# Performance work log

Hardware: AMD Instinct MI355X
Metric: run time of the kernel (lower is better)

Reference implementation:

```python
import jax, jax.numpy as jnp
import numpy as np

D_HIDDEN = 1024
N_HEADS = 16
D_HEAD = 64
B, N = 4, 1024
EPS = 1e-5


def _lin(x, w, b):
    # torch Linear: y = x @ W^T + b, w: [out, in]
    return jnp.einsum('...i,oi->...o', x, w) + b


def _ln(x, g, b):
    m = jnp.mean(x, axis=-1, keepdims=True)
    v = jnp.mean(jnp.square(x - m), axis=-1, keepdims=True)
    return (x - m) * jax.lax.rsqrt(v + EPS) * g + b


def setup_inputs() -> dict:
    key = jax.random.key(0)
    ks = jax.random.split(key, 20)
    d = D_HIDDEN
    s = 0.02
    inp = {
        'x': jax.random.normal(ks[0], (B, N, d), jnp.float32),
        'time_emb': jax.random.normal(ks[1], (B, d), jnp.float32),
        'ln1_g': jnp.ones((d,), jnp.float32),
        'ln1_b': jnp.zeros((d,), jnp.float32),
        's1_w': jax.random.normal(ks[2], (d, d), jnp.float32) * s,
        's1_b': jnp.zeros((d,), jnp.float32),
        'o1_w': jax.random.normal(ks[3], (d, d), jnp.float32) * s,
        'o1_b': jnp.zeros((d,), jnp.float32),
        'qkv_w': jax.random.normal(ks[4], (3 * d, d), jnp.float32) * s,
        'qkv_b': jnp.zeros((3 * d,), jnp.float32),
        'proj_w': jax.random.normal(ks[5], (d, d), jnp.float32) * s,
        'proj_b': jnp.zeros((d,), jnp.float32),
        'ln2_g': jnp.ones((d,), jnp.float32),
        'ln2_b': jnp.zeros((d,), jnp.float32),
        's2_w': jax.random.normal(ks[6], (d, d), jnp.float32) * s,
        's2_b': jnp.zeros((d,), jnp.float32),
        'o2_w': jax.random.normal(ks[7], (d, d), jnp.float32) * s,
        'o2_b': jnp.zeros((d,), jnp.float32),
        'up_w': jax.random.normal(ks[8], (4 * d, d), jnp.float32) * s,
        'up_b': jnp.zeros((4 * d,), jnp.float32),
        'down_w': jax.random.normal(ks[9], (d, 4 * d), jnp.float32) * s,
        'down_b': jnp.zeros((d,), jnp.float32),
    }
    return inp


def reference(x, time_emb, ln1_g, ln1_b, s1_w, s1_b, o1_w, o1_b,
              qkv_w, qkv_b, proj_w, proj_b, ln2_g, ln2_b,
              s2_w, s2_b, o2_w, o2_b, up_w, up_b, down_w, down_b):
    d = D_HIDDEN

    def ada(h, sw, sb, ow, ob):
        scale = _lin(time_emb, sw, sb)[:, None, :]   # [B,1,d]
        offset = _lin(time_emb, ow, ob)[:, None, :]
        return (1.0 + scale) * h + offset

    # attention branch
    h = ada(_ln(x, ln1_g, ln1_b), s1_w, s1_b, o1_w, o1_b)
    qkv = _lin(h, qkv_w, qkv_b)                       # [B,N,3d]
    q, k, v = jnp.split(qkv, 3, axis=-1)
    q = q.reshape(B, N, N_HEADS, D_HEAD)
    k = k.reshape(B, N, N_HEADS, D_HEAD)
    v = v.reshape(B, N, N_HEADS, D_HEAD)
    wei = jnp.einsum('bnhd,bmhd->bhnm', q, k) * (D_HEAD ** -0.5)
    wei = jax.nn.softmax(wei, axis=-1)
    attn = jnp.einsum('bhnm,bmhd->bnhd', wei, v).reshape(B, N, d)
    x = x + _lin(attn, proj_w, proj_b)

    # mlp branch (torch nn.GELU default = exact erf gelu)
    h = ada(_ln(x, ln2_g, ln2_b), s2_w, s2_b, o2_w, o2_b)
    h = jax.nn.gelu(_lin(h, up_w, up_b), approximate=False)
    x = x + _lin(h, down_w, down_b)
    return x, time_emb
```

## Files before the change

kernel.cpp:

```cpp
#include <hip/hip_runtime.h>
#include <hip/hip_bf16.h>
#include <math.h>

#define DH 1024
#define BB 4
#define NN 1024
#define NH 16
#define HD 64

typedef __attribute__((ext_vector_type(8))) short bf16x8;
typedef __attribute__((ext_vector_type(4))) float f32x4;
typedef unsigned short u16;

static __device__ __forceinline__ u16 f2bf(float f) {
  __hip_bfloat16 h = __float2bfloat16(f);
  return *reinterpret_cast<u16*>(&h);
}

#define MFMA16(a, b, c) __builtin_amdgcn_mfma_f32_16x16x32_bf16(a, b, c, 0, 0, 0)
#define VMCNT(n) asm volatile("s_waitcnt vmcnt(" #n ")" ::: "memory")
#define MEMFENCE asm volatile("" ::: "memory")

static __device__ __forceinline__ void async16(const void* g, void* l) {
  __builtin_amdgcn_global_load_lds(
      (const __attribute__((address_space(1))) void*)g,
      (__attribute__((address_space(3))) void*)l, 16, 0, 0);
}

__global__ void cvt_all_kernel(const float* __restrict__ wq, const float* __restrict__ wp,
                               const float* __restrict__ wu, const float* __restrict__ wd,
                               u16* __restrict__ oq, u16* __restrict__ op,
                               u16* __restrict__ ou, u16* __restrict__ od) {
  int i = blockIdx.x * 256 + threadIdx.x;
  const float* src; u16* dst; int off;
  if (i < 786432)            { src = wq; dst = oq; off = i; }
  else if (i < 1048576)      { src = wp; dst = op; off = i - 786432; }
  else if (i < 2097152)      { src = wu; dst = ou; off = i - 1048576; }
  else                       { src = wd; dst = od; off = i - 2097152; }
  float4 v = reinterpret_cast<const float4*>(src)[off];
  ushort4 o;
  o.x = f2bf(v.x); o.y = f2bf(v.y); o.z = f2bf(v.z); o.w = f2bf(v.w);
  reinterpret_cast<ushort4*>(dst)[off] = o;
}

__global__ __launch_bounds__(256) void adaln_kernel(
    const float* __restrict__ e,
    const float* __restrict__ w_s1, const float* __restrict__ b_s1,
    const float* __restrict__ w_o1, const float* __restrict__ b_o1,
    const float* __restrict__ w_s2, const float* __restrict__ b_s2,
    const float* __restrict__ w_o2, const float* __restrict__ b_o2,
    float* __restrict__ out) {
  int tid = threadIdx.x, wid = tid >> 6, lane = tid & 63;
  int mat = blockIdx.y;
  const float* w; const float* bs; float addc;
  if (mat == 0)      { w = w_s1; bs = b_s1; addc = 1.f; }
  else if (mat == 1) { w = w_o1; bs = b_o1; addc = 0.f; }
  else if (mat == 2) { w = w_s2; bs = b_s2; addc = 1.f; }
  else               { w = w_o2; bs = b_o2; addc = 0.f; }
  int col = blockIdx.x * 4 + wid;
  float a0 = 0.f, a1 = 0.f, a2 = 0.f, a3 = 0.f;
  const float* wc_ = w + (size_t)col * DH;
  for (int i = 0; i < 16; ++i) {
    int k = i * 64 + lane;
    float wv = wc_[k];
    a0 += wv * e[k];
    a1 += wv * e[DH + k];
    a2 += wv * e[2 * DH + k];
    a3 += wv * e[3 * DH + k];
  }
  #pragma unroll
  for (int msk = 32; msk; msk >>= 1) {
    a0 += __shfl_xor(a0, msk); a1 += __shfl_xor(a1, msk);
    a2 += __shfl_xor(a2, msk); a3 += __shfl_xor(a3, msk);
  }
  if (lane == 0) {
    float bb = bs[col] + addc;
    out[mat * (4 * DH) + 0 * DH + col] = a0 + bb;
    out[mat * (4 * DH) + 1 * DH + col] = a1 + bb;
    out[mat * (4 * DH) + 2 * DH + col] = a2 + bb;
    out[mat * (4 * DH) + 3 * DH + col] = a3 + bb;
  }
}

__global__ __launch_bounds__(256) void ln_mod_kernel(
    const float* __restrict__ x, const float* __restrict__ g, const float* __restrict__ bta,
    const float* __restrict__ sp, const float* __restrict__ off, u16* __restrict__ out) {
  int row = blockIdx.x;
  int b = row >> 10;
  int tid = threadIdx.x;
  int wid = tid >> 6, lane = tid & 63;
  const float4 xv = reinterpret_cast<const float4*>(x + (size_t)row * DH)[tid];
  float s = xv.x + xv.y + xv.z + xv.w;
  float ss = xv.x * xv.x + xv.y * xv.y + xv.z * xv.z + xv.w * xv.w;
  #pragma unroll
  for (int m = 32; m; m >>= 1) { s += __shfl_xor(s, m); ss += __shfl_xor(ss, m); }
  __shared__ float red[8];
  if (lane == 0) { red[wid] = s; red[4 + wid] = ss; }
  __syncthreads();
  s = red[0] + red[1] + red[2] + red[3];
  ss = red[4] + red[5] + red[6] + red[7];
  float mean = s * (1.f / DH);
  float var = ss * (1.f / DH) - mean * mean;
  float rstd = rsqrtf(var + 1e-5f);
  int c = tid * 4;
  const float* spb = sp + b * DH + c;
  const float* offb = off + b * DH + c;
  float y0 = (xv.x - mean) * rstd * g[c + 0] + bta[c + 0];
  float y1 = (xv.y - mean) * rstd * g[c + 1] + bta[c + 1];
  float y2 = (xv.z - mean) * rstd * g[c + 2] + bta[c + 2];
  float y3 = (xv.w - mean) * rstd * g[c + 3] + bta[c + 3];
  ushort4 o;
  o.x = f2bf(spb[0] * y0 + offb[0]);
  o.y = f2bf(spb[1] * y1 + offb[1]);
  o.z = f2bf(spb[2] * y2 + offb[2]);
  o.w = f2bf(spb[3] * y3 + offb[3]);
  reinterpret_cast<ushort4*>(out + (size_t)row * DH)[tid] = o;
}

enum { EPI_BF16 = 0, EPI_GELU = 1, EPI_F32PART = 2 };

template <int EPI>
__global__ __launch_bounds__(512, 2) void gemm256_kernel(
    const u16* __restrict__ A, const u16* __restrict__ W,
    const float* __restrict__ bias, void* __restrict__ outp,
    int N, int K, int KT) {
  extern __shared__ u16 lds[];
  u16* Ab = lds;
  u16* Bb = lds + 32768;
  int tid = threadIdx.x;
  int wid = tid >> 6, lane = tid & 63;
  int l15 = lane & 15, l4 = lane >> 4;
  int wr = wid >> 2, wc = wid & 3;

  int nwg = gridDim.x * gridDim.y;
  int lin = blockIdx.y * gridDim.x + blockIdx.x;
  int q8 = nwg >> 3;
  int lin2 = (lin & 7) * q8 + (lin >> 3);
  int bx = lin2 % gridDim.x, by = lin2 / gridDim.x;
  int m0 = by * 256, n0 = bx * 256;
  int k0 = blockIdx.z * (KT << 5);

  f32x4 acc[8][4] = {};

  const u16* Abase = A + (size_t)m0 * K + k0;
  const u16* Wbase = W + (size_t)n0 * K + k0;
  int i0 = tid, i1 = 512 + tid;
  int r0 = i0 >> 2, c0 = (i0 & 3) ^ ((r0 >> 1) & 3);
  int r1 = i1 >> 2, c1 = (i1 & 3) ^ ((r1 >> 1) & 3);
  size_t gO0 = (size_t)r0 * K + c0 * 8;
  size_t gO1 = (size_t)r1 * K + c1 * 8;
  int lb0 = (wid * 64) * 8;
  int lb1 = (512 + wid * 64) * 8;

  auto stage = [&](int tt) {
    int q = (tt & 3) * 8192;
    const u16* Ak = Abase + tt * 32;
    const u16* Wk = Wbase + tt * 32;
    async16(Ak + gO0, &Ab[q + lb0]);
    async16(Ak + gO1, &Ab[q + lb1]);
    async16(Wk + gO0, &Bb[q + lb0]);
    async16(Wk + gO1, &Bb[q + lb1]);
  };

  auto compute = [&](int tt) {
    int q = (tt & 3) * 8192;
    bf16x8 af[8], bfr[4];
    #pragma unroll
    for (int m = 0; m < 8; ++m) {
      int row = wr * 128 + m * 16 + l15;
      int ps = l4 ^ ((row >> 1) & 3);
      af[m] = *reinterpret_cast<const bf16x8*>(&Ab[q + row * 32 + ps * 8]);
    }
    #pragma unroll
    for (int n = 0; n < 4; ++n) {
      int row = wc * 64 + n * 16 + l15;
      int ps = l4 ^ ((row >> 1) & 3);
      bfr[n] = *reinterpret_cast<const bf16x8*>(&Bb[q + row * 32 + ps * 8]);
    }
    #pragma unroll
    for (int m = 0; m < 8; ++m)
      #pragma unroll
      for (int n = 0; n < 4; ++n)
        acc[m][n] = MFMA16(af[m], bfr[n], acc[m][n]);
  };

  stage(0);
  if (KT > 1) stage(1);
  if (KT > 2) stage(2);
  for (int t = 0; t < KT; ++t) {
    if (t < KT - 3) { stage(t + 3); VMCNT(12); }
    else if (t == KT - 3) { VMCNT(8); }
    else if (t == KT - 2) { VMCNT(4); }
    else { VMCNT(0); }
    __builtin_amdgcn_s_barrier();
    MEMFENCE;
    compute(t);
    MEMFENCE;
    __builtin_amdgcn_s_barrier();
  }

  int M = gridDim.y * 256;
  float* fout = (float*)outp + (size_t)blockIdx.z * M * N;
  #pragma unroll
  for (int n = 0; n < 4; ++n) {
    int col = n0 + wc * 64 + n * 16 + l15;
    float bv = (EPI == EPI_F32PART) ? 0.f : bias[col];
    #pragma unroll
    for (int m = 0; m < 8; ++m) {
      #pragma unroll
      for (int r = 0; r < 4; ++r) {
        int rowg = m0 + wr * 128 + m * 16 + l4 * 4 + r;
        float v = acc[m][n][r] + bv;
        if (EPI == EPI_GELU) {
          v = 0.5f * v * (1.f + erff(v * 0.70710678118f));
          ((u16*)outp)[(size_t)rowg * N + col] = f2bf(v);
        } else if (EPI == EPI_BF16) {
          ((u16*)outp)[(size_t)rowg * N + col] = f2bf(v);
        } else {
          fout[(size_t)rowg * N + col] = v;
        }
      }
    }
  }
}

enum { OEPI_BF16 = 0, OEPI_GELU = 1, OEPI_RES = 2 };

template <int EPI>
__global__ __launch_bounds__(256, 3) void gemm_bt_kernel(
    const u16* __restrict__ A, const u16* __restrict__ W,
    const float* __restrict__ bias, const float* __restrict__ resid,
    void* __restrict__ outp, int N, int K) {
  __shared__ __align__(16) u16 As[2][128 * 32];
  __shared__ __align__(16) u16 Ws[2][128 * 32];
  int tid = threadIdx.x;
  int wid = tid >> 6, lane = tid & 63;
  int l15 = lane & 15, l4 = lane >> 4;
  int m0 = blockIdx.y * 128, n0 = blockIdx.x * 128;
  int wr = wid >> 1, wc = wid & 1;
  f32x4 acc[4][4] = {};

  const int KT = K >> 5;
  int idx0 = tid, idx1 = 256 + tid;
  int rowA0 = idx0 >> 2, gs0 = (idx0 & 3) ^ ((rowA0 >> 1) & 3);
  int rowA1 = idx1 >> 2, gs1 = (idx1 & 3) ^ ((rowA1 >> 1) & 3);
  const u16* Abase = A + (size_t)m0 * K;
  const u16* Wbase = W + (size_t)n0 * K;
  int lb0 = (wid * 64) * 8;
  int lb1 = (256 + wid * 64) * 8;

  auto stage = [&](int buf, int kt) {
    const u16* Ak = Abase + kt * 32;
    const u16* Wk = Wbase + kt * 32;
    async16(Ak + (size_t)rowA0 * K + gs0 * 8, &As[buf][lb0]);
    async16(Wk + (size_t)rowA0 * K + gs0 * 8, &Ws[buf][lb0]);
    async16(Ak + (size_t)rowA1 * K + gs1 * 8, &As[buf][lb1]);
    async16(Wk + (size_t)rowA1 * K + gs1 * 8, &Ws[buf][lb1]);
  };

  auto compute = [&](int buf) {
    bf16x8 af[4], wf[4];
    #pragma unroll
    for (int m = 0; m < 4; ++m) {
      int row = wr * 64 + m * 16 + l15;
      int ps = l4 ^ ((row >> 1) & 3);
      af[m] = *reinterpret_cast<const bf16x8*>(&As[buf][row * 32 + ps * 8]);
    }
    #pragma unroll
    for (int n = 0; n < 4; ++n) {
      int row = wc * 64 + n * 16 + l15;
      int ps = l4 ^ ((row >> 1) & 3);
      wf[n] = *reinterpret_cast<const bf16x8*>(&Ws[buf][row * 32 + ps * 8]);
    }
    #pragma unroll
    for (int m = 0; m < 4; ++m)
      #pragma unroll
      for (int n = 0; n < 4; ++n)
        acc[m][n] = MFMA16(af[m], wf[n], acc[m][n]);
  };

  stage(0, 0);
  __syncthreads();
  int buf = 0;
  for (int kt = 0; kt < KT - 1; ++kt) {
    stage(buf ^ 1, kt + 1);
    compute(buf);
    __syncthreads();
    buf ^= 1;
  }
  compute(buf);

  #pragma unroll
  for (int n = 0; n < 4; ++n) {
    int col = n0 + wc * 64 + n * 16 + l15;
    float bv = bias[col];
    #pragma unroll
    for (int m = 0; m < 4; ++m) {
      #pragma unroll
      for (int r = 0; r < 4; ++r) {
        int rowg = m0 + wr * 64 + m * 16 + l4 * 4 + r;
        float v = acc[m][n][r] + bv;
        if (EPI == OEPI_GELU) {
          v = 0.5f * v * (1.f + erff(v * 0.70710678118f));
          ((u16*)outp)[(size_t)rowg * N + col] = f2bf(v);
        } else if (EPI == OEPI_BF16) {
          ((u16*)outp)[(size_t)rowg * N + col] = f2bf(v);
        } else {
          ((float*)outp)[(size_t)rowg * N + col] = v + resid[(size_t)rowg * N + col];
        }
      }
    }
  }
}

__global__ __launch_bounds__(256) void reduce4_kernel(
    const float* __restrict__ part, const float* __restrict__ x2,
    const float* __restrict__ bias, float* __restrict__ out) {
  size_t i = (size_t)blockIdx.x * 256 + threadIdx.x;
  const size_t MN4 = (size_t)4096 * 1024 / 4;
  float4 a0 = reinterpret_cast<const float4*>(part)[i];
  float4 a1 = reinterpret_cast<const float4*>(part)[i + MN4];
  float4 a2 = reinterpret_cast<const float4*>(part)[i + 2 * MN4];
  float4 a3 = reinterpret_cast<const float4*>(part)[i + 3 * MN4];
  float4 xr = reinterpret_cast<const float4*>(x2)[i];
  int col = (int)((i * 4) & 1023);
  float4 bv = *reinterpret_cast<const float4*>(&bias[col]);
  float4 o;
  o.x = xr.x + bv.x + a0.x + a1.x + a2.x + a3.x;
  o.y = xr.y + bv.y + a0.y + a1.y + a2.y + a3.y;
  o.z = xr.z + bv.z + a0.z + a1.z + a2.z + a3.z;
  o.w = xr.w + bv.w + a0.w + a1.w + a2.w + a3.w;
  reinterpret_cast<float4*>(out)[i] = o;
}

__global__ __launch_bounds__(256, 4) void attn_kernel(
    const u16* __restrict__ qkv, u16* __restrict__ out) {
  __shared__ __align__(16) u16 Ks[2][4096];
  __shared__ __align__(16) u16 Vt[2][4096];
  __shared__ __align__(16) u16 Ps[4][1024];
  int tid = threadIdx.x, wid = tid >> 6, lane = tid & 63;
  int l15 = lane & 15, l4 = lane >> 4;
  int L = blockIdx.y * gridDim.x + blockIdx.x;
  int qt = (L >> 3) & 15;
  int bh = (L & 7) | ((L >> 7) << 3);
  int b = bh >> 4, h = bh & 15;
  const size_t SN = 3 * DH;
  const u16* qb = qkv + (size_t)b * NN * SN + h * HD;
  const u16* kb = qb + DH;
  const u16* vb = qb + 2 * DH;

  int qrow = qt * 64 + wid * 16 + l15;
  bf16x8 qf[2];
  #pragma unroll
  for (int ks = 0; ks < 2; ++ks)
    qf[ks] = *reinterpret_cast<const bf16x8*>(qb + (size_t)qrow * SN + ks * 32 + l4 * 8);

  float m_[4], l_[4];
  f32x4 o_[4] = {};
  #pragma unroll
  for (int r = 0; r < 4; ++r) { m_[r] = -1e30f; l_[r] = 0.f; }

  int iA = tid, iB = 256 + tid;
  int jA = iA >> 3, sA = iA & 7, gsA = sA ^ (jA & 7);
  int jB = iB >> 3, sB = iB & 7, gsB = sB ^ (jB & 7);

  auto vwrite = [&](int bufn, bf16x8 v0, bf16x8 v1) {
    #pragma unroll
    for (int e = 0; e < 8; ++e) {
      int d = sA * 8 + e;
      int ps = (jA >> 3) ^ (d & 7) ^ ((d >> 3) & 7);
      Vt[bufn][d * 64 + ps * 8 + (jA & 7)] = v0[e];
      int d2 = sB * 8 + e;
      int ps2 = (jB >> 3) ^ (d2 & 7) ^ ((d2 >> 3) & 7);
      Vt[bufn][d2 * 64 + ps2 * 8 + (jB & 7)] = v1[e];
    }
  };

  {
    async16(kb + (size_t)jA * SN + gsA * 8, &Ks[0][iA * 8]);
    async16(kb + (size_t)jB * SN + gsB * 8, &Ks[0][iB * 8]);
    bf16x8 v0 = *reinterpret_cast<const bf16x8*>(vb + (size_t)jA * SN + sA * 8);
    bf16x8 v1 = *reinterpret_cast<const bf16x8*>(vb + (size_t)jB * SN + sB * 8);
    vwrite(0, v0, v1);
    __syncthreads();
  }

  int buf = 0;
  for (int t = 0; t < 16; ++t) {
    bf16x8 vna, vnb;
    if (t < 15) {
      const u16* kt = kb + (size_t)(t + 1) * 64 * SN;
      const u16* vt = vb + (size_t)(t + 1) * 64 * SN;
      async16(kt + (size_t)jA * SN + gsA * 8, &Ks[buf ^ 1][iA * 8]);
      async16(kt + (size_t)jB * SN + gsB * 8, &Ks[buf ^ 1][iB * 8]);
      vna = *reinterpret_cast<const bf16x8*>(vt + (size_t)jA * SN + sA * 8);
      vnb = *reinterpret_cast<const bf16x8*>(vt + (size_t)jB * SN + sB * 8);
    }

    f32x4 sa[4];
    #pragma unroll
    for (int nb = 0; nb < 4; ++nb) {
      f32x4 s = {};
      #pragma unroll
      for (int ks = 0; ks < 2; ++ks) {
        int j = nb * 16 + l15;
        int ps = (ks * 4 + l4) ^ (j & 7);
        bf16x8 kf = *reinterpret_cast<const bf16x8*>(&Ks[buf][j * 64 + ps * 8]);
        s = MFMA16(qf[ks], kf, s);
      }
      sa[nb] = s * 0.125f;
    }

    float corr[4], tsum[4];
    #pragma unroll
    for (int r = 0; r < 4; ++r) {
      float v = fmaxf(fmaxf(sa[0][r], sa[1][r]), fmaxf(sa[2][r], sa[3][r]));
      #pragma unroll
      for (int msk = 1; msk < 16; msk <<= 1) v = fmaxf(v, __shfl_xor(v, msk));
      float mn = fmaxf(m_[r], v);
      corr[r] = __expf(m_[r] - mn);
      m_[r] = mn;
      tsum[r] = 0.f;
    }
    #pragma unroll
    for (int nb = 0; nb < 4; ++nb) {
      #pragma unroll
      for (int r = 0; r < 4; ++r) {
        float p = __expf(sa[nb][r] - m_[r]);
        sa[nb][r] = p;
        tsum[r] += p;
      }
    }
    #pragma unroll
    for (int r = 0; r < 4; ++r) {
      float v = tsum[r];
      #pragma unroll
      for (int msk = 1; msk < 16; msk <<= 1) v += __shfl_xor(v, msk);
      l_[r] = l_[r] * corr[r] + v;
    }
    #pragma unroll
    for (int nd = 0; nd < 4; ++nd) {
      #pragma unroll
      for (int r = 0; r < 4; ++r) o_[nd][r] *= corr[r];
    }

    u16* Pw = Ps[wid];
    #pragma unroll
    for (int nb = 0; nb < 4; ++nb) {
      int slot = nb * 2 + (l15 >> 3);
      #pragma unroll
      for (int r = 0; r < 4; ++r) {
        int row = l4 * 4 + r;
        int ps = slot ^ (row & 7);
        Pw[row * 64 + ps * 8 + (l15 & 7)] = f2bf(sa[nb][r]);
      }
    }

    __builtin_amdgcn_s_setprio(1);
    #pragma unroll
    for (int ks = 0; ks < 2; ++ks) {
      int psp = (ks * 4 + l4) ^ (l15 & 7);
      bf16x8 pa = *reinterpret_cast<const bf16x8*>(&Pw[l15 * 64 + psp * 8]);
      #pragma unroll
      for (int nd = 0; nd < 4; ++nd) {
        int d = nd * 16 + l15;
        int psv = (ks * 4 + l4) ^ (d & 7) ^ ((d >> 3) & 7);
        bf16x8 vf = *reinterpret_cast<const bf16x8*>(&Vt[buf][d * 64 + psv * 8]);
        o_[nd] = MFMA16(pa, vf, o_[nd]);
      }
    }
    __builtin_amdgcn_s_setprio(0);

    if (t < 15) {
      vwrite(buf ^ 1, vna, vnb);
      __syncthreads();
    }
    buf ^= 1;
  }

  float inv[4];
  #pragma unroll
  for (int r = 0; r < 4; ++r) inv[r] = 1.f / l_[r];
  u16* ob = out + (size_t)b * NN * DH + h * HD;
  #pragma unroll
  for (int nd = 0; nd < 4; ++nd) {
    #pragma unroll
    for (int r = 0; r < 4; ++r) {
      int q = qt * 64 + wid * 16 + l4 * 4 + r;
      ob[(size_t)q * DH + nd * 16 + l15] = f2bf(o_[nd][r] * inv[r]);
    }
  }
}

__global__ void copy_te_kernel(const float* __restrict__ te, float* __restrict__ out) {
  int i = blockIdx.x * blockDim.x + threadIdx.x;
  if (i < BB * DH) out[i] = te[i];
}

extern "C" void kernel_launch(void* const* d_in, const int* in_sizes, int n_in,
                              void* d_out, int out_size, void* d_ws, size_t ws_size,
                              hipStream_t stream) {
  (void)in_sizes; (void)n_in; (void)out_size; (void)ws_size;
  const float* x      = (const float*)d_in[0];
  const float* te     = (const float*)d_in[1];
  const float* ln1_g  = (const float*)d_in[2];
  const float* ln1_b  = (const float*)d_in[3];
  const float* s1_w   = (const float*)d_in[4];
  const float* s1_b   = (const float*)d_in[5];
  const float* o1_w   = (const float*)d_in[6];
  const float* o1_b   = (const float*)d_in[7];
  const float* qkv_w  = (const float*)d_in[8];
  const float* qkv_b  = (const float*)d_in[9];
  const float* proj_w = (const float*)d_in[10];
  const float* proj_b = (const float*)d_in[11];
  const float* ln2_g  = (const float*)d_in[12];
  const float* ln2_b  = (const float*)d_in[13];
  const float* s2_w   = (const float*)d_in[14];
  const float* s2_b   = (const float*)d_in[15];
  const float* o2_w   = (const float*)d_in[16];
  const float* o2_b   = (const float*)d_in[17];
  const float* up_w   = (const float*)d_in[18];
  const float* up_b   = (const float*)d_in[19];
  const float* down_w = (const float*)d_in[20];
  const float* down_b = (const float*)d_in[21];

  char* ws = (char*)d_ws;
  size_t off = 0;
  auto alloc = [&](size_t bytes) { void* p = ws + off; off += (bytes + 255) & ~255ull; return p; };
  u16*   wq   = (u16*)  alloc((size_t)3072 * 1024 * 2);
  u16*   wp   = (u16*)  alloc((size_t)1024 * 1024 * 2);
  u16*   wu   = (u16*)  alloc((size_t)4096 * 1024 * 2);
  u16*   h1   = (u16*)  alloc((size_t)4096 * 1024 * 2);
  u16*   qkvb = (u16*)  alloc((size_t)4096 * 3072 * 2);
  u16*   att  = (u16*)  alloc((size_t)4096 * 1024 * 2);
  u16*   h2   = (u16*)  alloc((size_t)4096 * 1024 * 2);
  u16*   wd   = (u16*)  alloc((size_t)1024 * 4096 * 2);
  float* x2   = (float*)alloc((size_t)4096 * 1024 * 4);
  u16*   upb  = (u16*)  alloc((size_t)4096 * 4096 * 2);
  float* ada  = (float*)alloc((size_t)4 * 4 * 1024 * 4);
  float* sp1 = ada, *off1 = ada + 4096, *sp2 = ada + 8192, *off2 = ada + 12288;
  float* part = (float*)wq;

  cvt_all_kernel<<<12288, 256, 0, stream>>>(qkv_w, proj_w, up_w, down_w, wq, wp, wu, wd);
  adaln_kernel<<<dim3(256, 4), 256, 0, stream>>>(te, s1_w, s1_b, o1_w, o1_b, s2_w, s2_b, o2_w, o2_b, ada);
  ln_mod_kernel<<<4096, 256, 0, stream>>>(x, ln1_g, ln1_b, sp1, off1, h1);
  gemm256_kernel<EPI_BF16><<<dim3(12, 16, 1), 512, 131072, stream>>>(h1, wq, qkv_b, qkvb, 3072, 1024, 32);
  attn_kernel<<<dim3(16, 64), 256, 0, stream>>>(qkvb, att);
  gemm_bt_kernel<OEPI_RES><<<dim3(8, 32), 256, 0, stream>>>(att, wp, proj_b, x, x2, 1024, 1024);
  ln_mod_kernel<<<4096, 256, 0, stream>>>(x2, ln2_g, ln2_b, sp2, off2, h2);
  gemm256_kernel<EPI_GELU><<<dim3(16, 16, 1), 512, 131072, stream>>>(h2, wu, up_b, upb, 4096, 1024, 32);
  gemm256_kernel<EPI_F32PART><<<dim3(4, 16, 4), 512, 131072, stream>>>(upb, wd, nullptr, part, 1024, 4096, 32);
  reduce4_kernel<<<4096, 256, 0, stream>>>(part, x2, down_b, (float*)d_out);
  copy_te_kernel<<<16, 256, 0, stream>>>(te, (float*)d_out + 4096 * 1024);
}
```

Measured before the change: 277.1 us.

## Pre-transpose V in a separate kernel, async-stage it, lazily rescale softmax

A new vt_kernel transposes V from the qkv buffer into a per-head [d][n] layout (reusing the h1 buffer). The attention kernel can then stage V into LDS with async global-to-LDS loads, like K, instead of register loads followed by scattered transposed LDS writes. The online softmax now rescales the running max, sum and output only when some row's max grows by more than 8 in a wavefront, which skips exp and multiply work on most tiles. The copy of time_emb is folded into the reduce kernel, removing one launch. The cost is an extra kernel launch and an extra global read and write of V.

Measured after the change: 274.1 us. About the same (-1.1%).

```diff
diff --git a/kernel.cpp b/kernel.cpp
--- a/kernel.cpp
+++ b/kernel.cpp
@@ -315,7 +315,8 @@
 
 __global__ __launch_bounds__(256) void reduce4_kernel(
     const float* __restrict__ part, const float* __restrict__ x2,
-    const float* __restrict__ bias, float* __restrict__ out) {
+    const float* __restrict__ bias, const float* __restrict__ te,
+    float* __restrict__ out) {
   size_t i = (size_t)blockIdx.x * 256 + threadIdx.x;
   const size_t MN4 = (size_t)4096 * 1024 / 4;
   float4 a0 = reinterpret_cast<const float4*>(part)[i];
@@ -331,12 +332,45 @@
   o.z = xr.z + bv.z + a0.z + a1.z + a2.z + a3.z;
   o.w = xr.w + bv.w + a0.w + a1.w + a2.w + a3.w;
   reinterpret_cast<float4*>(out)[i] = o;
+  if (blockIdx.x < 16) {
+    int ii = blockIdx.x * 256 + threadIdx.x;
+    out[4096 * 1024 + ii] = te[ii];
+  }
+}
+
+__global__ __launch_bounds__(256) void vt_kernel(const u16* __restrict__ qkvb,
+                                                 u16* __restrict__ vT) {
+  __shared__ u16 L[64 * 66];
+  int bh = blockIdx.y;
+  int b = bh >> 4, h = bh & 15;
+  int nt = blockIdx.x;
+  int t = threadIdx.x;
+  const u16* src = qkvb + ((size_t)b * 1024 + nt * 64) * 3072 + 2048 + h * 64;
+  int j = t >> 3, s = t & 7;
+  bf16x8 r0 = *reinterpret_cast<const bf16x8*>(src + (size_t)j * 3072 + s * 8);
+  bf16x8 r1 = *reinterpret_cast<const bf16x8*>(src + (size_t)(j + 32) * 3072 + s * 8);
+  #pragma unroll
+  for (int e = 0; e < 8; ++e) {
+    L[(s * 8 + e) * 66 + j] = r0[e];
+    L[(s * 8 + e) * 66 + j + 32] = r1[e];
+  }
+  __syncthreads();
+  int d = t & 63, cp = t >> 6;
+  u16* dst = vT + ((size_t)bh * 64 + d) * 1024 + nt * 64;
+  #pragma unroll
+  for (int half = 0; half < 2; ++half) {
+    int cs = cp + half * 4;
+    bf16x8 o;
+    #pragma unroll
+    for (int c = 0; c < 8; ++c) o[c] = L[d * 66 + cs * 8 + c];
+    *reinterpret_cast<bf16x8*>(dst + cs * 8) = o;
+  }
 }
 
 __global__ __launch_bounds__(256, 4) void attn_kernel(
-    const u16* __restrict__ qkv, u16* __restrict__ out) {
+    const u16* __restrict__ qkv, const u16* __restrict__ vT, u16* __restrict__ out) {
   __shared__ __align__(16) u16 Ks[2][4096];
-  __shared__ __align__(16) u16 Vt[2][4096];
+  __shared__ __align__(16) u16 Vs[2][4096];
   __shared__ __align__(16) u16 Ps[4][1024];
   int tid = threadIdx.x, wid = tid >> 6, lane = tid & 63;
   int l15 = lane & 15, l4 = lane >> 4;
@@ -347,7 +381,7 @@
   const size_t SN = 3 * DH;
   const u16* qb = qkv + (size_t)b * NN * SN + h * HD;
   const u16* kb = qb + DH;
-  const u16* vb = qb + 2 * DH;
+  const u16* vtb = vT + (size_t)bh * 64 * 1024;
 
   int qrow = qt * 64 + wid * 16 + l15;
   bf16x8 qf[2];
@@ -364,38 +398,21 @@
   int jA = iA >> 3, sA = iA & 7, gsA = sA ^ (jA & 7);
   int jB = iB >> 3, sB = iB & 7, gsB = sB ^ (jB & 7);
 
-  auto vwrite = [&](int bufn, bf16x8 v0, bf16x8 v1) {
-    #pragma unroll
-    for (int e = 0; e < 8; ++e) {
-      int d = sA * 8 + e;
-      int ps = (jA >> 3) ^ (d & 7) ^ ((d >> 3) & 7);
-      Vt[bufn][d * 64 + ps * 8 + (jA & 7)] = v0[e];
-      int d2 = sB * 8 + e;
-      int ps2 = (jB >> 3) ^ (d2 & 7) ^ ((d2 >> 3) & 7);
-      Vt[bufn][d2 * 64 + ps2 * 8 + (jB & 7)] = v1[e];
-    }
+  auto stageKV = [&](int bufn, int t) {
+    const u16* kt = kb + (size_t)t * 64 * SN;
+    async16(kt + (size_t)jA * SN + gsA * 8, &Ks[bufn][iA * 8]);
+    async16(kt + (size_t)jB * SN + gsB * 8, &Ks[bufn][iB * 8]);
+    const u16* vt = vtb + (size_t)t * 64;
+    async16(vt + (size_t)jA * 1024 + gsA * 8, &Vs[bufn][iA * 8]);
+    async16(vt + (size_t)jB * 1024 + gsB * 8, &Vs[bufn][iB * 8]);
   };
 
-  {
-    async16(kb + (size_t)jA * SN + gsA * 8, &Ks[0][iA * 8]);
-    async16(kb + (size_t)jB * SN + gsB * 8, &Ks[0][iB * 8]);
-    bf16x8 v0 = *reinterpret_cast<const bf16x8*>(vb + (size_t)jA * SN + sA * 8);
-    bf16x8 v1 = *reinterpret_cast<const bf16x8*>(vb + (size_t)jB * SN + sB * 8);
-    vwrite(0, v0, v1);
-    __syncthreads();
-  }
+  stageKV(0, 0);
+  __syncthreads();
 
   int buf = 0;
   for (int t = 0; t < 16; ++t) {
-    bf16x8 vna, vnb;
-    if (t < 15) {
-      const u16* kt = kb + (size_t)(t + 1) * 64 * SN;
-      const u16* vt = vb + (size_t)(t + 1) * 64 * SN;
-      async16(kt + (size_t)jA * SN + gsA * 8, &Ks[buf ^ 1][iA * 8]);
-      async16(kt + (size_t)jB * SN + gsB * 8, &Ks[buf ^ 1][iB * 8]);
-      vna = *reinterpret_cast<const bf16x8*>(vt + (size_t)jA * SN + sA * 8);
-      vnb = *reinterpret_cast<const bf16x8*>(vt + (size_t)jB * SN + sB * 8);
-    }
+    if (t < 15) stageKV(buf ^ 1, t + 1);
 
     f32x4 sa[4];
     #pragma unroll
@@ -411,17 +428,29 @@
       sa[nb] = s * 0.125f;
     }
 
-    float corr[4], tsum[4];
+    float rm[4], tsum[4];
     #pragma unroll
     for (int r = 0; r < 4; ++r) {
       float v = fmaxf(fmaxf(sa[0][r], sa[1][r]), fmaxf(sa[2][r], sa[3][r]));
       #pragma unroll
       for (int msk = 1; msk < 16; msk <<= 1) v = fmaxf(v, __shfl_xor(v, msk));
-      float mn = fmaxf(m_[r], v);
-      corr[r] = __expf(m_[r] - mn);
-      m_[r] = mn;
-      tsum[r] = 0.f;
-    }
+      rm[r] = v;
+    }
+    float gmx = fmaxf(fmaxf(rm[0] - m_[0], rm[1] - m_[1]),
+                      fmaxf(rm[2] - m_[2], rm[3] - m_[3]));
+    if (!__all(gmx <= 8.f)) {
+      #pragma unroll
+      for (int r = 0; r < 4; ++r) {
+        float mn = fmaxf(m_[r], rm[r]);
+        float corr = __expf(m_[r] - mn);
+        m_[r] = mn;
+        l_[r] *= corr;
+        #pragma unroll
+        for (int nd = 0; nd < 4; ++nd) o_[nd][r] *= corr;
+      }
+    }
+    #pragma unroll
+    for (int r = 0; r < 4; ++r) tsum[r] = 0.f;
     #pragma unroll
     for (int nb = 0; nb < 4; ++nb) {
       #pragma unroll
@@ -436,12 +465,7 @@
       float v = tsum[r];
       #pragma unroll
       for (int msk = 1; msk < 16; msk <<= 1) v += __shfl_xor(v, msk);
-      l_[r] = l_[r] * corr[r] + v;
-    }
-    #pragma unroll
-    for (int nd = 0; nd < 4; ++nd) {
-      #pragma unroll
-      for (int r = 0; r < 4; ++r) o_[nd][r] *= corr[r];
+      l_[r] += v;
     }
 
     u16* Pw = Ps[wid];
@@ -464,17 +488,14 @@
       #pragma unroll
       for (int nd = 0; nd < 4; ++nd) {
         int d = nd * 16 + l15;
-        int psv = (ks * 4 + l4) ^ (d & 7) ^ ((d >> 3) & 7);
-        bf16x8 vf = *reinterpret_cast<const bf16x8*>(&Vt[buf][d * 64 + psv * 8]);
+        int psv = (ks * 4 + l4) ^ (d & 7);
+        bf16x8 vf = *reinterpret_cast<const bf16x8*>(&Vs[buf][d * 64 + psv * 8]);
         o_[nd] = MFMA16(pa, vf, o_[nd]);
       }
     }
     __builtin_amdgcn_s_setprio(0);
 
-    if (t < 15) {
-      vwrite(buf ^ 1, vna, vnb);
-      __syncthreads();
-    }
+    if (t < 15) __syncthreads();
     buf ^= 1;
   }
 
@@ -490,11 +511,6 @@
       ob[(size_t)q * DH + nd * 16 + l15] = f2bf(o_[nd][r] * inv[r]);
     }
   }
-}
-
-__global__ void copy_te_kernel(const float* __restrict__ te, float* __restrict__ out) {
-  int i = blockIdx.x * blockDim.x + threadIdx.x;
-  if (i < BB * DH) out[i] = te[i];
 }
 
 extern "C" void kernel_launch(void* const* d_in, const int* in_sizes, int n_in,
@@ -540,16 +556,17 @@
   float* ada  = (float*)alloc((size_t)4 * 4 * 1024 * 4);
   float* sp1 = ada, *off1 = ada + 4096, *sp2 = ada + 8192, *off2 = ada + 12288;
   float* part = (float*)wq;
+  u16*   vT   = h1;
 
   cvt_all_kernel<<<12288, 256, 0, stream>>>(qkv_w, proj_w, up_w, down_w, wq, wp, wu, wd);
   adaln_kernel<<<dim3(256, 4), 256, 0, stream>>>(te, s1_w, s1_b, o1_w, o1_b, s2_w, s2_b, o2_w, o2_b, ada);
   ln_mod_kernel<<<4096, 256, 0, stream>>>(x, ln1_g, ln1_b, sp1, off1, h1);
   gemm256_kernel<EPI_BF16><<<dim3(12, 16, 1), 512, 131072, stream>>>(h1, wq, qkv_b, qkvb, 3072, 1024, 32);
-  attn_kernel<<<dim3(16, 64), 256, 0, stream>>>(qkvb, att);
+  vt_kernel<<<dim3(16, 64), 256, 0, stream>>>(qkvb, vT);
+  attn_kernel<<<dim3(16, 64), 256, 0, stream>>>(qkvb, vT, att);
   gemm_bt_kernel<OEPI_RES><<<dim3(8, 32), 256, 0, stream>>>(att, wp, proj_b, x, x2, 1024, 1024);
   ln_mod_kernel<<<4096, 256, 0, stream>>>(x2, ln2_g, ln2_b, sp2, off2, h2);
   gemm256_kernel<EPI_GELU><<<dim3(16, 16, 1), 512, 131072, stream>>>(h2, wu, up_b, upb, 4096, 1024, 32);
   gemm256_kernel<EPI_F32PART><<<dim3(4, 16, 4), 512, 131072, stream>>>(upb, wd, nullptr, part, 1024, 4096, 32);
-  reduce4_kernel<<<4096, 256, 0, stream>>>(part, x2, down_b, (float*)d_out);
-  copy_te_kernel<<<16, 256, 0, stream>>>(te, (float*)d_out + 4096 * 1024);
-}
+  reduce4_kernel<<<4096, 256, 0, stream>>>(part, x2, down_b, te, (float*)d_out);
+}
```
